# Optimization experiments

Hardware: AMD Instinct MI355X
Metric: run time of the kernel (lower is better)

## Reference

```python
import jax, jax.numpy as jnp
import numpy as np

B, L, H, P, A, T = 64, 256, 1024, 64, 512, 8


def setup_inputs() -> dict:
    key = jax.random.key(0)
    ks = jax.random.split(key, 9)
    return {
        "word_hiddens": jax.random.normal(ks[0], (B, L, H), dtype=jnp.float32),
        "pos_e1_embeddings": jax.random.normal(ks[1], (B, L, P), dtype=jnp.float32),
        "pos_e2_embeddings": jax.random.normal(ks[2], (B, L, P), dtype=jnp.float32),
        "e1_end": jax.random.randint(ks[3], (B,), 0, L, dtype=jnp.int32),
        "e2_end": jax.random.randint(ks[4], (B,), 0, L, dtype=jnp.int32),
        "type_embeddings": jax.random.normal(ks[5], (T, H), dtype=jnp.float32) * 0.03,
        "W_pos": jax.random.normal(ks[6], (H + 2 * P, A), dtype=jnp.float32) * 0.03,
        "W_ent": jax.random.normal(ks[7], (4 * H, A), dtype=jnp.float32) * 0.02,
        "v": jax.random.normal(ks[8], (A,), dtype=jnp.float32) * 0.05,
    }


def _latent_type(e_h, type_emb):
    # alpha = softmax(e_h @ C^T); latent type = alpha @ C   (C: [T, latent])
    scores = jnp.einsum("bh,th->bt", e_h, type_emb)
    alpha = jax.nn.softmax(scores, axis=-1)
    return jnp.einsum("bt,th->bh", alpha, type_emb)


def reference(word_hiddens, pos_e1_embeddings, pos_e2_embeddings, e1_end, e2_end,
              type_embeddings, W_pos, W_ent, v):
    b, seq_len, h = word_hiddens.shape
    batch_idx = jnp.arange(b)
    e1_h = word_hiddens[batch_idx, e1_end]          # [B, H]
    e2_h = word_hiddens[batch_idx, e2_end]          # [B, H]
    e1_type = _latent_type(e1_h, type_embeddings)   # [B, H]
    e2_type = _latent_type(e2_h, type_embeddings)   # [B, H]

    entity_features = jnp.concatenate([e1_h, e1_type, e2_h, e2_type], axis=-1)  # [B, 4H]
    pos_features = jnp.concatenate([word_hiddens, pos_e1_embeddings, pos_e2_embeddings], axis=-1)  # [B, L, H+2P]

    dense_pos = jnp.einsum("blf,fa->bla", pos_features, W_pos)   # [B, L, A]
    dense_ent = entity_features @ W_ent                          # [B, A]
    # Faithful to original tf.repeat(axis=1)+reshape (element-interleaved, not a broadcast)
    dense_ent_r = jnp.repeat(dense_ent, seq_len, axis=1).reshape(b, seq_len, -1)  # [B, L, A]

    u = jnp.tanh(dense_pos + dense_ent_r)            # [B, L, A]
    vu = jnp.einsum("bla,a->bl", u, v)               # [B, L]
    alpha = jax.nn.softmax(vu, axis=-1)              # [B, L]
    z = jnp.einsum("blh,bl->bh", word_hiddens, alpha)  # [B, H]
    return z
```

## Files before the change

kernel.cpp:

```cpp
#include <hip/hip_runtime.h>
#include <hip/hip_bf16.h>
#include <math.h>

#define B_ 64
#define L_ 256
#define H_ 1024
#define P_ 64
#define A_ 512
#define T_ 8
#define NSTEP 36

#define AS1 __attribute__((address_space(1)))
#define AS3 __attribute__((address_space(3)))

typedef __attribute__((ext_vector_type(8))) __bf16 bf16x8;
typedef __attribute__((ext_vector_type(4))) float f32x4;

__device__ __forceinline__ float bf2f(ushort u) {
  union { unsigned int i; float f; } v; v.i = ((unsigned int)u) << 16; return v.f;
}
__device__ __forceinline__ ushort f2bf_rne(float f) {
  union { float f; unsigned int i; } v; v.f = f;
  unsigned int r = v.i + 0x7FFFu + ((v.i >> 16) & 1u);
  return (ushort)(r >> 16);
}
__device__ __forceinline__ unsigned int pack2_rne(float a, float b) {
  return (unsigned int)f2bf_rne(a) | ((unsigned int)f2bf_rne(b) << 16);
}

template <bool BF16>
__device__ __forceinline__ float ld1(const void* p, size_t i) {
  if (BF16) return bf2f(((const ushort*)p)[i]);
  return ((const float*)p)[i];
}
template <bool BF16>
__device__ __forceinline__ float2 ld2(const void* p, size_t i) {
  if (BF16) {
    ushort2 u = *(const ushort2*)((const ushort*)p + i);
    return (float2){bf2f(u.x), bf2f(u.y)};
  }
  return *(const float2*)((const float*)p + i);
}
template <bool BF16>
__device__ __forceinline__ float4 ld4(const void* p, size_t i) {
  if (BF16) {
    ushort4 u = *(const ushort4*)((const ushort*)p + i);
    return (float4){bf2f(u.x), bf2f(u.y), bf2f(u.z), bf2f(u.w)};
  }
  return *(const float4*)((const float*)p + i);
}

__device__ __forceinline__ void gll16(const void* g, void* l) {
  __builtin_amdgcn_global_load_lds((const AS1 void*)g, (AS3 void*)l, 16, 0, 0);
}

__device__ __forceinline__ void barrier_nodrain() {
  __builtin_amdgcn_sched_barrier(0);
  asm volatile("s_waitcnt lgkmcnt(0)" ::: "memory");
  __builtin_amdgcn_sched_barrier(0);
  __builtin_amdgcn_s_barrier();
  __builtin_amdgcn_sched_barrier(0);
}

template <bool BF16>
__global__ __launch_bounds__(256) void prep_k(
    const void* __restrict__ wpos, ushort* __restrict__ WTs,
    const void* __restrict__ wh, const int* __restrict__ e1e,
    const int* __restrict__ e2e, const void* __restrict__ temb,
    float* __restrict__ EF) {
  if (blockIdx.x < 576) {
    __shared__ ushort tile[32][33];
    const int s  = blockIdx.x >> 4;
    const int at = blockIdx.x & 15;
    const int tx = threadIdx.x & 31;
    const int ty = threadIdx.x >> 5;
#pragma unroll
    for (int i = 0; i < 4; ++i) {
      size_t idx = (size_t)(s * 32 + ty + i * 8) * A_ + at * 32 + tx;
      ushort u;
      if (BF16) u = ((const ushort*)wpos)[idx];
      else u = f2bf_rne(((const float*)wpos)[idx]);
      tile[ty + i * 8][tx] = u;
    }
    __syncthreads();
#pragma unroll
    for (int i = 0; i < 4; ++i) {
      WTs[(size_t)s * (A_ * 32) + (size_t)(at * 32 + ty + i * 8) * 32 + tx] =
          tile[tx][ty + i * 8];
    }
  } else {
    const int b = blockIdx.x - 576;
    const int tid = threadIdx.x;
    __shared__ float eh1[1024];
    __shared__ float eh2[1024];
    __shared__ float part[256][16];
    __shared__ float part2[16][17];
    __shared__ float scores[16];
    __shared__ float alpha[16];

    const size_t o1 = ((size_t)b * L_ + e1e[b]) * H_;
    const size_t o2 = ((size_t)b * L_ + e2e[b]) * H_;
    for (int h = tid; h < 1024; h += 256) {
      eh1[h] = ld1<BF16>(wh, o1 + h);
      eh2[h] = ld1<BF16>(wh, o2 + h);
    }
    __syncthreads();

    float p[16];
#pragma unroll
    for (int t = 0; t < 16; ++t) p[t] = 0.f;
    for (int h = tid; h < 1024; h += 256) {
      float a1 = eh1[h], a2 = eh2[h];
#pragma unroll
      for (int t = 0; t < 8; ++t) {
        float c = ld1<BF16>(temb, t * 1024 + h);
        p[t] += a1 * c;
        p[8 + t] += a2 * c;
      }
    }
#pragma unroll
    for (int t = 0; t < 16; ++t) part[tid][t] = p[t];
    __syncthreads();
    {
      const int t = tid & 15, j = tid >> 4;
      float s = 0.f;
#pragma unroll
      for (int i = 0; i < 16; ++i) s += part[j * 16 + i][t];
      part2[j][t] = s;
    }
    __syncthreads();
    if (tid < 16) {
      float s = 0.f;
#pragma unroll
      for (int i = 0; i < 16; ++i) s += part2[i][tid];
      scores[tid] = s;
    }
    __syncthreads();
    if (tid < 2) {
      const int base = tid * 8;
      float mx = scores[base];
      for (int t = 1; t < 8; ++t) mx = fmaxf(mx, scores[base + t]);
      float sum = 0.f;
      float e[8];
      for (int t = 0; t < 8; ++t) { e[t] = __expf(scores[base + t] - mx); sum += e[t]; }
      float inv = 1.f / sum;
      for (int t = 0; t < 8; ++t) alpha[base + t] = e[t] * inv;
    }
    __syncthreads();

    float* efb = EF + (size_t)b * 4096;
    for (int h = tid; h < 1024; h += 256) {
      float l1 = 0.f, l2 = 0.f;
#pragma unroll
      for (int t = 0; t < 8; ++t) {
        float c = ld1<BF16>(temb, t * 1024 + h);
        l1 += alpha[t] * c;
        l2 += alpha[8 + t] * c;
      }
      efb[h] = eh1[h];
      efb[1024 + h] = l1;
      efb[2048 + h] = eh2[h];
      efb[3072 + h] = l2;
    }
  }
}

template <bool BF16>
__global__ __launch_bounds__(256) void ent_gemm(const float* __restrict__ EF,
                                                const void* __restrict__ went,
                                                float* __restrict__ part) {
  const int mh = blockIdx.x & 1;
  const int nb = (blockIdx.x >> 1) & 3;
  const int kb = blockIdx.x >> 3;
  const int tid = threadIdx.x;
  __shared__ float efs[32][128];

  const int k0 = kb * 128;
  {
    const int kq = (tid & 31) * 4;
    for (int m = tid >> 5; m < 32; m += 8) {
      *(float4*)&efs[m][kq] = *(const float4*)&EF[(size_t)(mh * 32 + m) * 4096 + k0 + kq];
    }
  }
  __syncthreads();

  const int n0 = nb * 128 + (tid & 31) * 4;
  const int mg = (tid >> 5) * 4;
  float acc[4][4];
#pragma unroll
  for (int i = 0; i < 4; ++i)
#pragma unroll
    for (int j = 0; j < 4; ++j) acc[i][j] = 0.f;

  for (int k = 0; k < 128; ++k) {
    float4 w = ld4<BF16>(went, (size_t)(k0 + k) * A_ + n0);
#pragma unroll
    for (int i = 0; i < 4; ++i) {
      float e = efs[mg + i][k];
      acc[i][0] += e * w.x;
      acc[i][1] += e * w.y;
      acc[i][2] += e * w.z;
      acc[i][3] += e * w.w;
    }
  }
#pragma unroll
  for (int i = 0; i < 4; ++i) {
    *(float4*)&part[((size_t)kb * 64 + mh * 32 + mg + i) * A_ + n0] =
        (float4){acc[i][0], acc[i][1], acc[i][2], acc[i][3]};
  }
}

__global__ __launch_bounds__(256) void ent_reduce(const float* __restrict__ part,
                                                  float* __restrict__ dense_ent) {
  const int idx = blockIdx.x * 256 + threadIdx.x;
  float s = 0.f;
#pragma unroll
  for (int kb = 0; kb < 32; ++kb) s += part[(size_t)kb * 32768 + idx];
  dense_ent[idx] = s;
}

__global__ __launch_bounds__(256, 4) void fused_gemm_vu_bf16(
    const ushort* __restrict__ wh, const ushort* __restrict__ pe1,
    const ushort* __restrict__ pe2, const ushort* __restrict__ WTs,
    const float* __restrict__ part, const ushort* __restrict__ vvec,
    float* __restrict__ vu_part) {
  __shared__ __align__(16) ushort Abuf[2][2048];
  __shared__ __align__(16) ushort Bbuf[2][4096];
  __shared__ float vu_s[4][64];
  __shared__ float dense_s[64];

  const int tid = threadIdx.x;
  const int pid = blockIdx.x;
  const int wid = (pid & 7) * 128 + (pid >> 3);
  const int nb = wid & 3;
  const int mb = wid >> 2;
  const int rbase = mb * 64;
  const int wave = tid >> 6;
  const int lane = tid & 63;
  const int quad = lane >> 4;
  const int col = lane & 15;
  const int wr = wave >> 1;
  const int wc = wave & 1;

  int aoff[2], boff[4];
#pragma unroll
  for (int mf = 0; mf < 2; ++mf) {
    const int ra = wr * 32 + mf * 16 + col;
    aoff[mf] = ra * 32 + ((quad ^ ((ra >> 1) & 3)) << 3);
  }
#pragma unroll
  for (int nf = 0; nf < 4; ++nf) {
    const int rb = wc * 64 + nf * 16 + col;
    boff[nf] = rb * 32 + ((quad ^ ((rb >> 1) & 3)) << 3);
  }

  const int srow = tid >> 2;
  const int csw = (((tid & 3) ^ ((srow >> 1) & 3)) << 3);
  const ushort* aw  = wh  + (size_t)(rbase + srow) * H_ + csw;
  const ushort* ap1 = pe1 + (size_t)(rbase + srow) * P_ + csw;
  const ushort* ap2 = pe2 + (size_t)(rbase + srow) * P_ + csw;
  const ushort* b1  = WTs + (size_t)(nb * 128 + srow) * 32 + csw;
  const ushort* b2  = WTs + (size_t)(nb * 128 + 64 + srow) * 32 + csw;

  auto stage = [&](int buf, int s) {
    const ushort* as;
    if (s < 32)      as = aw + s * 32;
    else if (s < 34) as = ap1 + (s - 32) * 32;
    else             as = ap2 + (s - 34) * 32;
    const size_t so = (size_t)s * (A_ * 32);
    gll16(as, &Abuf[buf][wave * 512]);
    gll16(b1 + so, &Bbuf[buf][wave * 512]);
    gll16(b2 + so, &Bbuf[buf][2048 + wave * 512]);
  };

  f32x4 acc[2][4];
#pragma unroll
  for (int i = 0; i < 2; ++i)
#pragma unroll
    for (int j = 0; j < 4; ++j) acc[i][j] = (f32x4){0.f, 0.f, 0.f, 0.f};

  const int bidx = rbase >> 8;
  float de = 0.f;
  if (tid < 64) {
    const int a = 2 * ((rbase & 255) + tid) + (nb >> 1);
#pragma unroll
    for (int kb = 0; kb < 32; ++kb)
      de += part[((size_t)kb * 64 + bidx) * A_ + a];
  }
  stage(0, 0);
  if (tid < 64) dense_s[tid] = de;
  __syncthreads();

  int buf = 0;
  for (int s = 0; s < NSTEP; ++s) {
    if (s + 1 < NSTEP) stage(buf ^ 1, s + 1);
    const ushort* Ab = Abuf[buf];
    const ushort* Bb = Bbuf[buf];
    bf16x8 af[2], bfr[4];
#pragma unroll
    for (int mf = 0; mf < 2; ++mf) af[mf] = *(const bf16x8*)&Ab[aoff[mf]];
#pragma unroll
    for (int nf = 0; nf < 4; ++nf) bfr[nf] = *(const bf16x8*)&Bb[boff[nf]];
#pragma unroll
    for (int mf = 0; mf < 2; ++mf)
#pragma unroll
      for (int nf = 0; nf < 4; ++nf)
        acc[mf][nf] =
            __builtin_amdgcn_mfma_f32_16x16x32_bf16(af[mf], bfr[nf], acc[mf][nf], 0, 0, 0);
    __syncthreads();
    buf ^= 1;
  }

  float vv[4];
#pragma unroll
  for (int nf = 0; nf < 4; ++nf)
    vv[nf] = bf2f(vvec[nb * 128 + wc * 64 + nf * 16 + col]);

#pragma unroll
  for (int mf = 0; mf < 2; ++mf) {
    const int row0 = wr * 32 + mf * 16 + quad * 4;
    const float e0 = dense_s[row0 + 0];
    const float e1 = dense_s[row0 + 1];
    const float e2 = dense_s[row0 + 2];
    const float e3 = dense_s[row0 + 3];
    float s0 = 0.f, s1 = 0.f, s2 = 0.f, s3 = 0.f;
#pragma unroll
    for (int nf = 0; nf < 4; ++nf) {
      float vn = vv[nf];
      s0 += tanhf(acc[mf][nf][0] + e0) * vn;
      s1 += tanhf(acc[mf][nf][1] + e1) * vn;
      s2 += tanhf(acc[mf][nf][2] + e2) * vn;
      s3 += tanhf(acc[mf][nf][3] + e3) * vn;
    }
    s0 += __shfl_xor(s0, 1); s0 += __shfl_xor(s0, 2); s0 += __shfl_xor(s0, 4); s0 += __shfl_xor(s0, 8);
    s1 += __shfl_xor(s1, 1); s1 += __shfl_xor(s1, 2); s1 += __shfl_xor(s1, 4); s1 += __shfl_xor(s1, 8);
    s2 += __shfl_xor(s2, 1); s2 += __shfl_xor(s2, 2); s2 += __shfl_xor(s2, 4); s2 += __shfl_xor(s2, 8);
    s3 += __shfl_xor(s3, 1); s3 += __shfl_xor(s3, 2); s3 += __shfl_xor(s3, 4); s3 += __shfl_xor(s3, 8);
    if (col == 0) {
      vu_s[wave][row0 + 0] = s0;
      vu_s[wave][row0 + 1] = s1;
      vu_s[wave][row0 + 2] = s2;
      vu_s[wave][row0 + 3] = s3;
    }
  }
  __syncthreads();
  if (tid < 64) {
    const int wrr = tid >> 5;
    float s = vu_s[wrr * 2][tid] + vu_s[wrr * 2 + 1][tid];
    vu_part[(size_t)nb * (B_ * L_) + rbase + tid] = s;
  }
}

__global__ __launch_bounds__(256, 4) void fused_gemm_vu_f32(
    const float* __restrict__ wh, const float* __restrict__ pe1,
    const float* __restrict__ pe2, const ushort* __restrict__ WTs,
    const float* __restrict__ dense_ent, const float* __restrict__ vvec,
    float* __restrict__ vu_part) {
  __shared__ __align__(16) ushort Abuf[2][64 * 32];
  __shared__ __align__(16) ushort Bbuf[2][128 * 32];
  __shared__ float vu_s[4][64];

  const int tid = threadIdx.x;
  const int pid = blockIdx.x;
  const int wid = (pid & 7) * 128 + (pid >> 3);
  const int nb = wid & 3;
  const int mb = wid >> 2;
  const int rbase = mb * 64;
  const int wave = tid >> 6;
  const int lane = tid & 63;
  const int quad = lane >> 4;
  const int col = lane & 15;
  const int wr = wave >> 1;
  const int wc = wave & 1;

  int aoff[2], boff[4];
#pragma unroll
  for (int mf = 0; mf < 2; ++mf) {
    const int ra = wr * 32 + mf * 16 + col;
    aoff[mf] = ra * 32 + ((quad ^ ((ra >> 1) & 3)) << 3);
  }
#pragma unroll
  for (int nf = 0; nf < 4; ++nf) {
    const int rb = wc * 64 + nf * 16 + col;
    boff[nf] = rb * 32 + ((quad ^ ((rb >> 1) & 3)) << 3);
  }

  const int brow = tid >> 1;
  const int bc0 = (tid & 1) * 2;
  const int sB0 = brow * 32 + ((bc0 ^ ((brow >> 1) & 3)) << 3);
  const size_t bsrc_off = (size_t)(nb * 128 + brow) * 32 + (size_t)(tid & 1) * 16;

  const int ar0 = tid >> 2, aq = tid & 3;
  const int sA0 = ar0 * 32 + ((aq ^ ((ar0 >> 1) & 3)) << 3);

  f32x4 acc[2][4];
#pragma unroll
  for (int i = 0; i < 2; ++i)
#pragma unroll
    for (int j = 0; j < 4; ++j) acc[i][j] = (f32x4){0.f, 0.f, 0.f, 0.f};

  float4 fXa, fXb; uint4 bX0, bX1;
  float4 fYa, fYb; uint4 bY0, bY1;

  auto ISSUE_X = [&](int s) {
    const float* src; int ld, k0;
    if (s < 32)      { src = wh;  ld = H_; k0 = s * 32; }
    else if (s < 34) { src = pe1; ld = P_; k0 = (s - 32) * 32; }
    else             { src = pe2; ld = P_; k0 = (s - 34) * 32; }
    const float* p0 = src + (size_t)(rbase + ar0) * ld + k0 + aq * 8;
    fXa = *(const float4*)p0;
    fXb = *(const float4*)(p0 + 4);
    const ushort* bs = WTs + (size_t)s * (A_ * 32) + bsrc_off;
    bX0 = *(const uint4*)bs;
    bX1 = *(const uint4*)(bs + 8);
  };
  auto ISSUE_Y = [&](int s) {
    const float* src; int ld, k0;
    if (s < 32)      { src = wh;  ld = H_; k0 = s * 32; }
    else if (s < 34) { src = pe1; ld = P_; k0 = (s - 32) * 32; }
    else             { src = pe2; ld = P_; k0 = (s - 34) * 32; }
    const float* p0 = src + (size_t)(rbase + ar0) * ld + k0 + aq * 8;
    fYa = *(const float4*)p0;
    fYb = *(const float4*)(p0 + 4);
    const ushort* bs = WTs + (size_t)s * (A_ * 32) + bsrc_off;
    bY0 = *(const uint4*)bs;
    bY1 = *(const uint4*)(bs + 8);
  };
  auto STORE_X = [&](int buf) {
    uint4 u0 = {pack2_rne(fXa.x, fXa.y), pack2_rne(fXa.z, fXa.w),
                pack2_rne(fXb.x, fXb.y), pack2_rne(fXb.z, fXb.w)};
    *(uint4*)&Abuf[buf][sA0] = u0;
    *(uint4*)&Bbuf[buf][sB0] = bX0;
    *(uint4*)&Bbuf[buf][sB0 ^ 8] = bX1;
  };
  auto STORE_Y = [&](int buf) {
    uint4 u0 = {pack2_rne(fYa.x, fYa.y), pack2_rne(fYa.z, fYa.w),
                pack2_rne(fYb.x, fYb.y), pack2_rne(fYb.z, fYb.w)};
    *(uint4*)&Abuf[buf][sA0] = u0;
    *(uint4*)&Bbuf[buf][sB0] = bY0;
    *(uint4*)&Bbuf[buf][sB0 ^ 8] = bY1;
  };
  auto COMPUTE = [&](int buf) {
    bf16x8 af[2], bfr[4];
#pragma unroll
    for (int mf = 0; mf < 2; ++mf) af[mf] = *(const bf16x8*)&Abuf[buf][aoff[mf]];
#pragma unroll
    for (int nf = 0; nf < 4; ++nf) bfr[nf] = *(const bf16x8*)&Bbuf[buf][boff[nf]];
#pragma unroll
    for (int mf = 0; mf < 2; ++mf)
#pragma unroll
      for (int nf = 0; nf < 4; ++nf)
        acc[mf][nf] =
            __builtin_amdgcn_mfma_f32_16x16x32_bf16(af[mf], bfr[nf], acc[mf][nf], 0, 0, 0);
  };

  ISSUE_X(0);
  ISSUE_Y(1);
  STORE_X(0);
  barrier_nodrain();

  for (int s = 0; s < NSTEP; s += 2) {
    if (s + 2 < NSTEP) ISSUE_X(s + 2);
    COMPUTE(0);
    STORE_Y(1);
    barrier_nodrain();
    if (s + 3 < NSTEP) ISSUE_Y(s + 3);
    COMPUTE(1);
    if (s + 2 < NSTEP) {
      STORE_X(0);
      barrier_nodrain();
    }
  }

  float vv[4];
#pragma unroll
  for (int nf = 0; nf < 4; ++nf)
    vv[nf] = vvec[nb * 128 + wc * 64 + nf * 16 + col];

#pragma unroll
  for (int mf = 0; mf < 2; ++mf) {
    const int row0 = wr * 32 + mf * 16 + quad * 4;
    const int r0 = rbase + row0;
    const int bidx = r0 >> 8;
    const int l0 = r0 & 255;
    const float* ebase = dense_ent + bidx * A_ + 2 * l0 + (nb >> 1);
    float e0 = ebase[0], e1 = ebase[2], e2 = ebase[4], e3 = ebase[6];
    float s0 = 0.f, s1 = 0.f, s2 = 0.f, s3 = 0.f;
#pragma unroll
    for (int nf = 0; nf < 4; ++nf) {
      float vn = vv[nf];
      s0 += tanhf(acc[mf][nf][0] + e0) * vn;
      s1 += tanhf(acc[mf][nf][1] + e1) * vn;
      s2 += tanhf(acc[mf][nf][2] + e2) * vn;
      s3 += tanhf(acc[mf][nf][3] + e3) * vn;
    }
    s0 += __shfl_xor(s0, 1); s0 += __shfl_xor(s0, 2); s0 += __shfl_xor(s0, 4); s0 += __shfl_xor(s0, 8);
    s1 += __shfl_xor(s1, 1); s1 += __shfl_xor(s1, 2); s1 += __shfl_xor(s1, 4); s1 += __shfl_xor(s1, 8);
    s2 += __shfl_xor(s2, 1); s2 += __shfl_xor(s2, 2); s2 += __shfl_xor(s2, 4); s2 += __shfl_xor(s2, 8);
    s3 += __shfl_xor(s3, 1); s3 += __shfl_xor(s3, 2); s3 += __shfl_xor(s3, 4); s3 += __shfl_xor(s3, 8);
    if (col == 0) {
      vu_s[wave][row0 + 0] = s0;
      vu_s[wave][row0 + 1] = s1;
      vu_s[wave][row0 + 2] = s2;
      vu_s[wave][row0 + 3] = s3;
    }
  }
  __syncthreads();
  if (tid < 64) {
    const int wrr = tid >> 5;
    float s = vu_s[wrr * 2][tid] + vu_s[wrr * 2 + 1][tid];
    vu_part[(size_t)nb * (B_ * L_) + rbase + tid] = s;
  }
}

template <bool BF16>
__global__ __launch_bounds__(256) void softmax_z(const void* __restrict__ wh,
                                                 const float* __restrict__ vu_part,
                                                 void* __restrict__ out) {
  const int b = blockIdx.x >> 1;
  const int hh = blockIdx.x & 1;
  const int tid = threadIdx.x;
  __shared__ float alpha[256];
  __shared__ float red[256];

  float x = 0.f;
#pragma unroll
  for (int p = 0; p < 4; ++p) x += vu_part[(size_t)p * (B_ * L_) + b * L_ + tid];
  red[tid] = x;
  __syncthreads();
  for (int s = 128; s > 0; s >>= 1) {
    if (tid < s) red[tid] = fmaxf(red[tid], red[tid + s]);
    __syncthreads();
  }
  float m = red[0];
  __syncthreads();
  float e = __expf(x - m);
  red[tid] = e;
  __syncthreads();
  for (int s = 128; s > 0; s >>= 1) {
    if (tid < s) red[tid] += red[tid + s];
    __syncthreads();
  }
  alpha[tid] = e / red[0];
  __syncthreads();

  const int h0 = hh * 512 + tid * 2;
  const size_t base = (size_t)b * L_ * H_ + h0;
  float z0 = 0.f, z1 = 0.f;
  for (int l = 0; l < 256; l += 8) {
    float2 u0 = ld2<BF16>(wh, base + (size_t)(l + 0) * H_);
    float2 u1 = ld2<BF16>(wh, base + (size_t)(l + 1) * H_);
    float2 u2 = ld2<BF16>(wh, base + (size_t)(l + 2) * H_);
    float2 u3 = ld2<BF16>(wh, base + (size_t)(l + 3) * H_);
    float2 u4 = ld2<BF16>(wh, base + (size_t)(l + 4) * H_);
    float2 u5 = ld2<BF16>(wh, base + (size_t)(l + 5) * H_);
    float2 u6 = ld2<BF16>(wh, base + (size_t)(l + 6) * H_);
    float2 u7 = ld2<BF16>(wh, base + (size_t)(l + 7) * H_);
    float a0 = alpha[l + 0], a1 = alpha[l + 1], a2 = alpha[l + 2], a3 = alpha[l + 3];
    float a4 = alpha[l + 4], a5 = alpha[l + 5], a6 = alpha[l + 6], a7 = alpha[l + 7];
    z0 += a0 * u0.x + a1 * u1.x + a2 * u2.x + a3 * u3.x
        + a4 * u4.x + a5 * u5.x + a6 * u6.x + a7 * u7.x;
    z1 += a0 * u0.y + a1 * u1.y + a2 * u2.y + a3 * u3.y
        + a4 * u4.y + a5 * u5.y + a6 * u6.y + a7 * u7.y;
  }
  if (BF16) {
    ((unsigned int*)out)[((size_t)b * H_ + h0) >> 1] = pack2_rne(z0, z1);
  } else {
    *(float2*)((float*)out + (size_t)b * H_ + h0) = (float2){z0, z1};
  }
}

extern "C" void kernel_launch(void* const* d_in, const int* in_sizes, int n_in,
                              void* d_out, int out_size, void* d_ws, size_t ws_size,
                              hipStream_t stream) {
  const void* wh   = d_in[0];
  const void* pe1  = d_in[1];
  const void* pe2  = d_in[2];
  const int*  e1e  = (const int*)d_in[3];
  const int*  e2e  = (const int*)d_in[4];
  const void* temb = d_in[5];
  const void* wpos = d_in[6];
  const void* went = d_in[7];
  const void* vvec = d_in[8];

  const bool bf16 = (in_sizes[0] == (int)(B_ * L_ * H_ * 2));

  char* ws = (char*)d_ws;
  ushort* WTs      = (ushort*)ws;
  float* dense_ent = (float*)(ws + 1179648);
  float* vu_part   = (float*)(ws + 1310720);
  float* EF        = (float*)(ws + 1310720);
  float* part      = (float*)(ws + 2359296);

  if (bf16) {
    prep_k<true ><<<dim3(640), dim3(256), 0, stream>>>(wpos, WTs, wh, e1e, e2e, temb, EF);
    ent_gemm<true ><<<dim3(256), dim3(256), 0, stream>>>(EF, went, part);
    fused_gemm_vu_bf16<<<dim3(1024), dim3(256), 0, stream>>>(
        (const ushort*)wh, (const ushort*)pe1, (const ushort*)pe2, WTs, part,
        (const ushort*)vvec, vu_part);
    softmax_z<true ><<<dim3(128), dim3(256), 0, stream>>>(wh, vu_part, d_out);
  } else {
    prep_k<false><<<dim3(640), dim3(256), 0, stream>>>(wpos, WTs, wh, e1e, e2e, temb, EF);
    ent_gemm<false><<<dim3(256), dim3(256), 0, stream>>>(EF, went, part);
    ent_reduce<<<dim3(128), dim3(256), 0, stream>>>(part, dense_ent);
    fused_gemm_vu_f32<<<dim3(1024), dim3(256), 0, stream>>>(
        (const float*)wh, (const float*)pe1, (const float*)pe2, WTs, dense_ent,
        (const float*)vvec, vu_part);
    softmax_z<false><<<dim3(128), dim3(256), 0, stream>>>(wh, vu_part, d_out);
  }
}
```

Measured before the change: 190.5 us.

## Load B tiles via global_load_lds and fold entity reduce into fused f32 GEMM

In the fp32 path, the W_pos tiles are now copied directly from global memory into LDS with global_load_lds. This replaces the register staging and explicit LDS stores, and the barriers use vmcnt-based waits so one stage of async loads can stay in flight. The separate ent_reduce launch is removed: each fused GEMM block sums the 32 partial entity products for its 64 rows into shared memory before the main loop. This saves a kernel launch and register pressure, but adds redundant partial-sum reads across the four column blocks and more complex wait-count bookkeeping.

After: 187.1 us. No clear change (-1.8%).

```diff
diff --git a/kernel.cpp b/kernel.cpp
--- a/kernel.cpp
+++ b/kernel.cpp
@@ -54,9 +54,16 @@
   __builtin_amdgcn_global_load_lds((const AS1 void*)g, (AS3 void*)l, 16, 0, 0);
 }
 
-__device__ __forceinline__ void barrier_nodrain() {
+__device__ __forceinline__ void bar_vm2() {
   __builtin_amdgcn_sched_barrier(0);
-  asm volatile("s_waitcnt lgkmcnt(0)" ::: "memory");
+  asm volatile("s_waitcnt vmcnt(2) lgkmcnt(0)" ::: "memory");
+  __builtin_amdgcn_sched_barrier(0);
+  __builtin_amdgcn_s_barrier();
+  __builtin_amdgcn_sched_barrier(0);
+}
+__device__ __forceinline__ void bar_vm0() {
+  __builtin_amdgcn_sched_barrier(0);
+  asm volatile("s_waitcnt vmcnt(0) lgkmcnt(0)" ::: "memory");
   __builtin_amdgcn_sched_barrier(0);
   __builtin_amdgcn_s_barrier();
   __builtin_amdgcn_sched_barrier(0);
@@ -210,15 +217,6 @@
   }
 }
 
-__global__ __launch_bounds__(256) void ent_reduce(const float* __restrict__ part,
-                                                  float* __restrict__ dense_ent) {
-  const int idx = blockIdx.x * 256 + threadIdx.x;
-  float s = 0.f;
-#pragma unroll
-  for (int kb = 0; kb < 32; ++kb) s += part[(size_t)kb * 32768 + idx];
-  dense_ent[idx] = s;
-}
-
 __global__ __launch_bounds__(256, 4) void fused_gemm_vu_bf16(
     const ushort* __restrict__ wh, const ushort* __restrict__ pe1,
     const ushort* __restrict__ pe2, const ushort* __restrict__ WTs,
@@ -354,11 +352,12 @@
 __global__ __launch_bounds__(256, 4) void fused_gemm_vu_f32(
     const float* __restrict__ wh, const float* __restrict__ pe1,
     const float* __restrict__ pe2, const ushort* __restrict__ WTs,
-    const float* __restrict__ dense_ent, const float* __restrict__ vvec,
+    const float* __restrict__ part, const float* __restrict__ vvec,
     float* __restrict__ vu_part) {
-  __shared__ __align__(16) ushort Abuf[2][64 * 32];
-  __shared__ __align__(16) ushort Bbuf[2][128 * 32];
+  __shared__ __align__(16) ushort Abuf[2][2048];
+  __shared__ __align__(16) ushort Bbuf[2][4096];
   __shared__ float vu_s[4][64];
+  __shared__ float dense_s[64];
 
   const int tid = threadIdx.x;
   const int pid = blockIdx.x;
@@ -385,10 +384,15 @@
     boff[nf] = rb * 32 + ((quad ^ ((rb >> 1) & 3)) << 3);
   }
 
-  const int brow = tid >> 1;
-  const int bc0 = (tid & 1) * 2;
-  const int sB0 = brow * 32 + ((bc0 ^ ((brow >> 1) & 3)) << 3);
-  const size_t bsrc_off = (size_t)(nb * 128 + brow) * 32 + (size_t)(tid & 1) * 16;
+  const int srow = tid >> 2;
+  const int csw = (((tid & 3) ^ ((srow >> 1) & 3)) << 3);
+  const ushort* b1 = WTs + (size_t)(nb * 128 + srow) * 32 + csw;
+  const ushort* b2 = WTs + (size_t)(nb * 128 + 64 + srow) * 32 + csw;
+  auto gllB = [&](int buf, int s) {
+    const size_t so = (size_t)s * (A_ * 32);
+    gll16(b1 + so, &Bbuf[buf][wave * 512]);
+    gll16(b2 + so, &Bbuf[buf][2048 + wave * 512]);
+  };
 
   const int ar0 = tid >> 2, aq = tid & 3;
   const int sA0 = ar0 * 32 + ((aq ^ ((ar0 >> 1) & 3)) << 3);
@@ -399,8 +403,8 @@
 #pragma unroll
     for (int j = 0; j < 4; ++j) acc[i][j] = (f32x4){0.f, 0.f, 0.f, 0.f};
 
-  float4 fXa, fXb; uint4 bX0, bX1;
-  float4 fYa, fYb; uint4 bY0, bY1;
+  float4 fXa, fXb;
+  float4 fYa, fYb;
 
   auto ISSUE_X = [&](int s) {
     const float* src; int ld, k0;
@@ -410,9 +414,6 @@
     const float* p0 = src + (size_t)(rbase + ar0) * ld + k0 + aq * 8;
     fXa = *(const float4*)p0;
     fXb = *(const float4*)(p0 + 4);
-    const ushort* bs = WTs + (size_t)s * (A_ * 32) + bsrc_off;
-    bX0 = *(const uint4*)bs;
-    bX1 = *(const uint4*)(bs + 8);
   };
   auto ISSUE_Y = [&](int s) {
     const float* src; int ld, k0;
@@ -422,23 +423,16 @@
     const float* p0 = src + (size_t)(rbase + ar0) * ld + k0 + aq * 8;
     fYa = *(const float4*)p0;
     fYb = *(const float4*)(p0 + 4);
-    const ushort* bs = WTs + (size_t)s * (A_ * 32) + bsrc_off;
-    bY0 = *(const uint4*)bs;
-    bY1 = *(const uint4*)(bs + 8);
   };
   auto STORE_X = [&](int buf) {
     uint4 u0 = {pack2_rne(fXa.x, fXa.y), pack2_rne(fXa.z, fXa.w),
                 pack2_rne(fXb.x, fXb.y), pack2_rne(fXb.z, fXb.w)};
     *(uint4*)&Abuf[buf][sA0] = u0;
-    *(uint4*)&Bbuf[buf][sB0] = bX0;
-    *(uint4*)&Bbuf[buf][sB0 ^ 8] = bX1;
   };
   auto STORE_Y = [&](int buf) {
     uint4 u0 = {pack2_rne(fYa.x, fYa.y), pack2_rne(fYa.z, fYa.w),
                 pack2_rne(fYb.x, fYb.y), pack2_rne(fYb.z, fYb.w)};
     *(uint4*)&Abuf[buf][sA0] = u0;
-    *(uint4*)&Bbuf[buf][sB0] = bY0;
-    *(uint4*)&Bbuf[buf][sB0 ^ 8] = bY1;
   };
   auto COMPUTE = [&](int buf) {
     bf16x8 af[2], bfr[4];
@@ -454,21 +448,37 @@
             __builtin_amdgcn_mfma_f32_16x16x32_bf16(af[mf], bfr[nf], acc[mf][nf], 0, 0, 0);
   };
 
+  const int bidx = rbase >> 8;
+  float de = 0.f;
+  if (tid < 64) {
+    const int a = 2 * ((rbase & 255) + tid) + (nb >> 1);
+#pragma unroll
+    for (int kb = 0; kb < 32; ++kb)
+      de += part[((size_t)kb * 64 + bidx) * A_ + a];
+  }
+  gllB(0, 0);
   ISSUE_X(0);
   ISSUE_Y(1);
   STORE_X(0);
-  barrier_nodrain();
+  if (tid < 64) dense_s[tid] = de;
+  __syncthreads();
 
   for (int s = 0; s < NSTEP; s += 2) {
+    gllB(1, s + 1);
+    __builtin_amdgcn_sched_barrier(0);
     if (s + 2 < NSTEP) ISSUE_X(s + 2);
     COMPUTE(0);
     STORE_Y(1);
-    barrier_nodrain();
-    if (s + 3 < NSTEP) ISSUE_Y(s + 3);
+    if (s + 2 < NSTEP) bar_vm2(); else bar_vm0();
+    if (s + 2 < NSTEP) {
+      gllB(0, s + 2);
+      __builtin_amdgcn_sched_barrier(0);
+      if (s + 3 < NSTEP) ISSUE_Y(s + 3);
+    }
     COMPUTE(1);
     if (s + 2 < NSTEP) {
       STORE_X(0);
-      barrier_nodrain();
+      if (s + 3 < NSTEP) bar_vm2(); else bar_vm0();
     }
   }
 
@@ -480,11 +490,10 @@
 #pragma unroll
   for (int mf = 0; mf < 2; ++mf) {
     const int row0 = wr * 32 + mf * 16 + quad * 4;
-    const int r0 = rbase + row0;
-    const int bidx = r0 >> 8;
-    const int l0 = r0 & 255;
-    const float* ebase = dense_ent + bidx * A_ + 2 * l0 + (nb >> 1);
-    float e0 = ebase[0], e1 = ebase[2], e2 = ebase[4], e3 = ebase[6];
+    const float e0 = dense_s[row0 + 0];
+    const float e1 = dense_s[row0 + 1];
+    const float e2 = dense_s[row0 + 2];
+    const float e3 = dense_s[row0 + 3];
     float s0 = 0.f, s1 = 0.f, s2 = 0.f, s3 = 0.f;
 #pragma unroll
     for (int nf = 0; nf < 4; ++nf) {
@@ -587,7 +596,6 @@
 
   char* ws = (char*)d_ws;
   ushort* WTs      = (ushort*)ws;
-  float* dense_ent = (float*)(ws + 1179648);
   float* vu_part   = (float*)(ws + 1310720);
   float* EF        = (float*)(ws + 1310720);
   float* part      = (float*)(ws + 2359296);
@@ -602,9 +610,8 @@
   } else {
     prep_k<false><<<dim3(640), dim3(256), 0, stream>>>(wpos, WTs, wh, e1e, e2e, temb, EF);
     ent_gemm<false><<<dim3(256), dim3(256), 0, stream>>>(EF, went, part);
-    ent_reduce<<<dim3(128), dim3(256), 0, stream>>>(part, dense_ent);
     fused_gemm_vu_f32<<<dim3(1024), dim3(256), 0, stream>>>(
-        (const float*)wh, (const float*)pe1, (const float*)pe2, WTs, dense_ent,
+        (const float*)wh, (const float*)pe1, (const float*)pe2, WTs, part,
         (const float*)vvec, vu_part);
     softmax_z<false><<<dim3(128), dim3(256), 0, stream>>>(wh, vu_part, d_out);
   }
```
